# Optimization experiments

Hardware: AMD Instinct MI355X
Metric: run time of the kernel (lower is better)

The kernel has to match this reference:

```python
import jax, jax.numpy as jnp
import numpy as np

B, S, D, H, F = 2, 1024, 2048, 16, 8192
DH = D // H
MAX_ALPHA = 0.2
CN_SCALE = D / (D - 1)  # CenterNorm scale factor dim/(dim-1)


def setup_inputs() -> dict:
    key = jax.random.key(0)
    ks = jax.random.split(key, 8)
    s = 0.02
    f32 = jnp.float32
    return {
        "x": jax.random.normal(ks[0], (B, S, D), f32),
        "ln1_g": jnp.ones((D,), f32), "ln1_b": jnp.zeros((D,), f32),
        "wq": jax.random.normal(ks[1], (D, D), f32) * s, "bq": jnp.zeros((D,), f32),
        "wk": jax.random.normal(ks[2], (D, D), f32) * s, "bk": jnp.zeros((D,), f32),
        "wv": jax.random.normal(ks[3], (D, D), f32) * s, "bv": jnp.zeros((D,), f32),
        "wo": jax.random.normal(ks[4], (D, D), f32) * s, "bo": jnp.zeros((D,), f32),
        "tau": jnp.ones((H,), f32),   # learnable per-head temperature, init_tau=1.0
        "nu": jnp.ones((H,), f32),    # learnable per-head output scale, init_nu=1.0
        "alpha1": jnp.full((D,), 0.1, f32),  # per-channel residual weight, init 0.1
        "ln2_g": jnp.ones((D,), f32), "ln2_b": jnp.zeros((D,), f32),
        "w1": jax.random.normal(ks[5], (F, D), f32) * s, "b1": jnp.zeros((F,), f32),
        "w2": jax.random.normal(ks[6], (D, F), f32) * s, "b2": jnp.zeros((D,), f32),
        "alpha2": jnp.full((D,), 0.1, f32),
    }


def _center_norm(x, g, b):
    # CenterNorm: subtract mean only (no variance), scale by dim/(dim-1)
    mu = jnp.mean(x, axis=-1, keepdims=True)
    return g * (CN_SCALE * (x - mu)) + b


def _l2norm(t):
    return t / (jnp.linalg.norm(t, axis=-1, keepdims=True) + 1e-6)


def _cosine_attn(x, wq, bq, wk, bk, wv, bv, wo, bo, tau, nu):
    # project and split heads -> [B,H,S,DH]
    def proj(w, b):
        return (jnp.einsum('bsd,ed->bse', x, w) + b).reshape(B, S, H, DH).transpose(0, 2, 1, 3)
    q, k, v = proj(wq, bq), proj(wk, bk), proj(wv, bv)
    qn, kn = _l2norm(q), _l2norm(k)  # cosine similarity attention
    scores = jnp.einsum('bhqd,bhkd->bhqk', qn, kn) * tau[None, :, None, None]
    causal = jnp.tril(jnp.ones((S, S), bool))
    scores = jnp.where(causal[None, None], scores, -jnp.inf)
    p = jax.nn.softmax(scores, axis=-1)
    o = jnp.einsum('bhqk,bhkd->bhqd', p, v) * nu[None, :, None, None]
    o = o.transpose(0, 2, 1, 3).reshape(B, S, D)
    return jnp.einsum('bsd,ed->bse', o, wo) + bo


def _ffn(x, w1, b1, w2, b2):
    h = jax.nn.gelu(jnp.einsum('bsd,fd->bsf', x, w1) + b1)
    return jnp.einsum('bsf,df->bsd', h, w2) + b2


def reference(x, ln1_g, ln1_b, wq, bq, wk, bk, wv, bv, wo, bo, tau, nu,
              alpha1, ln2_g, ln2_b, w1, b1, w2, b2, alpha2):
    a = _center_norm(x, ln1_g, ln1_b)
    a1 = jnp.clip(alpha1, -MAX_ALPHA, MAX_ALPHA)
    x1 = a + a1 * _cosine_attn(a, wq, bq, wk, bk, wv, bv, wo, bo, tau, nu)
    m = _center_norm(x1, ln2_g, ln2_b)
    a2 = jnp.clip(alpha2, -MAX_ALPHA, MAX_ALPHA)
    return m + a2 * _ffn(m, w1, b1, w2, b2)
```

## Files before the change

### kernel.cpp

```cpp
#include <hip/hip_runtime.h>
#include <hip/hip_bf16.h>
#include <stdint.h>

#define B_ 2
#define S_ 1024
#define D_ 2048
#define H_ 16
#define F_ 8192
#define DH_ 128
#define M_ 2048

typedef unsigned short u16;
typedef __attribute__((ext_vector_type(8))) short short8;
typedef __attribute__((ext_vector_type(4))) float f32x4;
typedef __attribute__((ext_vector_type(2))) float f32x2;
typedef __attribute__((ext_vector_type(2))) unsigned short u16x2;

__device__ __forceinline__ u16 f2bf(float f) {
  union { float f; uint32_t u; } c; c.f = f;
  uint32_t r = c.u + 0x7FFFu + ((c.u >> 16) & 1u);
  return (u16)(r >> 16);
}

__device__ __forceinline__ void gload16(const void* g, void* l) {
  __builtin_amdgcn_global_load_lds((const __attribute__((address_space(1))) void*)g,
                                   (__attribute__((address_space(3))) void*)l, 16, 0, 0);
}

__device__ __forceinline__ float clipa(float a) {
  return fminf(0.2f, fmaxf(-0.2f, a));
}

__device__ __forceinline__ float gelu_f(float x) {
  float z = 0.7978845608028654f * (x + 0.044715f * x * x * x);
  z = fminf(10.f, fmaxf(-10.f, z));
  float e = __expf(2.f * z);
  return 0.5f * x * (1.f + (e - 1.f) / (e + 1.f));
}

__global__ __launch_bounds__(256) void k_cvt_all(const float* __restrict__ wq,
                                                 const float* __restrict__ wk,
                                                 const float* __restrict__ wv,
                                                 const float* __restrict__ wo,
                                                 const float* __restrict__ w1,
                                                 const float* __restrict__ w2,
                                                 u16* __restrict__ dst) {
  const int gi = blockIdx.x * 256 + threadIdx.x;
  const float* s;
  int off;
  if (gi < 2097152) {
    int r = gi >> 19;
    s = r == 0 ? wq : (r == 1 ? wk : (r == 2 ? wv : wo));
    off = gi & 524287;
  } else if (gi < 4194304) {
    s = w1; off = gi - 2097152;
  } else {
    s = w2; off = gi - 4194304;
  }
  f32x4 a = *(const f32x4*)(s + (size_t)off * 8);
  f32x4 b = *(const f32x4*)(s + (size_t)off * 8 + 4);
  short8 o;
  o[0] = (short)f2bf(a[0]); o[1] = (short)f2bf(a[1]);
  o[2] = (short)f2bf(a[2]); o[3] = (short)f2bf(a[3]);
  o[4] = (short)f2bf(b[0]); o[5] = (short)f2bf(b[1]);
  o[6] = (short)f2bf(b[2]); o[7] = (short)f2bf(b[3]);
  *(short8*)(dst + (size_t)gi * 8) = o;
}

__global__ __launch_bounds__(256) void k_centernorm(const float* __restrict__ x,
                                                    const float* __restrict__ g,
                                                    const float* __restrict__ bb,
                                                    float* __restrict__ of,
                                                    u16* __restrict__ ob) {
  const int row = blockIdx.x;
  const int t = threadIdx.x;
  const float* xr = x + (size_t)row * D_;
  f32x4 v0 = *(const f32x4*)(xr + t * 8);
  f32x4 v1 = *(const f32x4*)(xr + t * 8 + 4);
  float s = v0[0] + v0[1] + v0[2] + v0[3] + v1[0] + v1[1] + v1[2] + v1[3];
#pragma unroll
  for (int off = 1; off < 64; off <<= 1) s += __shfl_xor(s, off);
  __shared__ float red[4];
  if ((t & 63) == 0) red[t >> 6] = s;
  __syncthreads();
  const float mu = (red[0] + red[1] + red[2] + red[3]) * (1.0f / D_);
  const float CNS = (float)D_ / (float)(D_ - 1);
  f32x4 g0 = *(const f32x4*)(g + t * 8);
  f32x4 g1 = *(const f32x4*)(g + t * 8 + 4);
  f32x4 b0 = *(const f32x4*)(bb + t * 8);
  f32x4 b1 = *(const f32x4*)(bb + t * 8 + 4);
  f32x4 y0, y1;
  short8 yb;
#pragma unroll
  for (int i = 0; i < 4; i++) {
    y0[i] = g0[i] * (CNS * (v0[i] - mu)) + b0[i];
    y1[i] = g1[i] * (CNS * (v1[i] - mu)) + b1[i];
  }
#pragma unroll
  for (int i = 0; i < 4; i++) { yb[i] = (short)f2bf(y0[i]); yb[4 + i] = (short)f2bf(y1[i]); }
  float* orow = of + (size_t)row * D_;
  *(f32x4*)(orow + t * 8) = y0;
  *(f32x4*)(orow + t * 8 + 4) = y1;
  *(short8*)(ob + (size_t)row * D_ + t * 8) = yb;
}

__global__ __launch_bounds__(256) void k_l2norm(const float* __restrict__ q,
                                                const float* __restrict__ k,
                                                const float* __restrict__ v,
                                                u16* __restrict__ qn,
                                                u16* __restrict__ kn,
                                                u16* __restrict__ vn) {
  const int gw = blockIdx.x * 4 + (threadIdx.x >> 6);
  const int l = threadIdx.x & 63;
  const int h = gw & (H_ - 1);
  const int s = (gw >> 4) & (S_ - 1);
  const int b = gw >> 14;
  const size_t src = ((size_t)(b * S_ + s)) * D_ + h * DH_ + l * 2;
  const size_t dst = (((size_t)(b * H_ + h)) * S_ + s) * DH_ + l * 2;
  {
    f32x2 xv = *(const f32x2*)(q + src);
    float ss = xv[0] * xv[0] + xv[1] * xv[1];
#pragma unroll
    for (int off = 1; off < 64; off <<= 1) ss += __shfl_xor(ss, off);
    float sc = 1.f / (sqrtf(ss) + 1e-6f);
    u16x2 o; o[0] = f2bf(xv[0] * sc); o[1] = f2bf(xv[1] * sc);
    *(u16x2*)(qn + dst) = o;
  }
  {
    f32x2 xv = *(const f32x2*)(k + src);
    float ss = xv[0] * xv[0] + xv[1] * xv[1];
#pragma unroll
    for (int off = 1; off < 64; off <<= 1) ss += __shfl_xor(ss, off);
    float sc = 1.f / (sqrtf(ss) + 1e-6f);
    u16x2 o; o[0] = f2bf(xv[0] * sc); o[1] = f2bf(xv[1] * sc);
    *(u16x2*)(kn + dst) = o;
  }
  {
    f32x2 xv = *(const f32x2*)(v + src);
    u16x2 o; o[0] = f2bf(xv[0]); o[1] = f2bf(xv[1]);
    *(u16x2*)(vn + dst) = o;
  }
}

template <int EPI>
__device__ __forceinline__ void gemm256_core(const u16* __restrict__ A,
                                             const u16* __restrict__ Bt,
                                             const float* __restrict__ bias,
                                             float* __restrict__ outf,
                                             u16* __restrict__ outb,
                                             int N, int K, int kbase, int nk,
                                             int m0, int n0) {
  __shared__ char lds[2][65536];
  const int t = threadIdx.x;
  const int l = t & 63, w = t >> 6;
  const int wr = w >> 2, wc = w & 3;
  const int l15 = l & 15, lhi = l >> 4;
  const int sw = (l15 & 7) << 4;
  const int ab0 = l15 * 128 + ((lhi * 16) ^ sw);
  const int ab1 = l15 * 128 + ((64 + lhi * 16) ^ sw);

  auto stage = [&](int kt, int h) {
#pragma unroll
    for (int rj = 0; rj < 4; rj++) {
      const int region = rj >> 1, j = rj & 1;
      const int pl = h * 16384 + j * 8192 + t * 16;
      const int row = pl >> 7;
      const int scol = (pl & 127) ^ ((row & 7) << 4);
      const int grow = (region ? n0 : m0) + row;
      const char* src = (const char*)(region ? Bt : A) +
                        (size_t)grow * (size_t)(K * 2) +
                        (size_t)((kbase + kt * 64) * 2 + scol);
      gload16(src, &lds[kt & 1][region * 32768 + pl]);
    }
  };

  f32x4 acc[8][4] = {};

  stage(0, 0); stage(0, 1); stage(1, 0);
  asm volatile("s_waitcnt vmcnt(4)" ::: "memory");
  __builtin_amdgcn_s_barrier();
  __builtin_amdgcn_sched_barrier(0);

  for (int kt = 0; kt < nk; ++kt) {
    const char* base = &lds[kt & 1][0];
    const char* pA0 = base + wr * 4096 + ab0;
    const char* pA1 = base + wr * 4096 + ab1;
    const char* pB0 = base + 32768 + wc * 8192 + ab0;
    const char* pB1 = base + 32768 + wc * 8192 + ab1;
    short8 bf[4][2];
#pragma unroll
    for (int ni = 0; ni < 4; ni++) {
      bf[ni][0] = *(const short8*)(pB0 + ni * 2048);
      bf[ni][1] = *(const short8*)(pB1 + ni * 2048);
    }
#pragma unroll
    for (int q = 0; q < 4; q++) {
      short8 aq[2][2];
#pragma unroll
      for (int mi = 0; mi < 2; mi++) {
        aq[mi][0] = *(const short8*)(pA0 + q * 8192 + mi * 2048);
        aq[mi][1] = *(const short8*)(pA1 + q * 8192 + mi * 2048);
      }
      if (q == 1 && kt + 1 < nk) stage(kt + 1, 1);
      if (q == 3 && kt + 2 < nk) stage(kt + 2, 0);
      __builtin_amdgcn_s_setprio(1);
#pragma unroll
      for (int ks = 0; ks < 2; ks++)
#pragma unroll
        for (int mi = 0; mi < 2; mi++)
#pragma unroll
          for (int ni = 0; ni < 4; ni++)
            acc[q * 2 + mi][ni] = __builtin_amdgcn_mfma_f32_16x16x32_bf16(
                aq[mi][ks], bf[ni][ks], acc[q * 2 + mi][ni], 0, 0, 0);
      __builtin_amdgcn_s_setprio(0);
      if (q == 1) __builtin_amdgcn_s_barrier();
    }
    if (kt + 1 < nk) {
      if (kt + 2 < nk) { asm volatile("s_waitcnt vmcnt(4)" ::: "memory"); }
      else             { asm volatile("s_waitcnt vmcnt(0)" ::: "memory"); }
      __builtin_amdgcn_s_barrier();
      __builtin_amdgcn_sched_barrier(0);
    }
  }

#pragma unroll
  for (int ni = 0; ni < 4; ni++) {
    const int col = n0 + wc * 64 + ni * 16 + l15;
    const float bcol = (EPI == 3) ? 0.f : bias[col];
#pragma unroll
    for (int ai = 0; ai < 8; ai++) {
      const int row = m0 + (ai >> 1) * 64 + wr * 32 + (ai & 1) * 16 + lhi * 4;
#pragma unroll
      for (int j = 0; j < 4; j++) {
        const float v = acc[ai][ni][j] + bcol;
        const size_t idx = (size_t)(row + j) * N + col;
        if (EPI == 0) outf[idx] = v;
        else if (EPI == 2) outb[idx] = f2bf(gelu_f(v));
        else outf[idx] = v;
      }
    }
  }
}

__global__ __launch_bounds__(512, 2) void k_qkv256(const u16* A, const u16* W,
                                                   const float* b0, const float* b1,
                                                   const float* b2, float* o0, float* o1,
                                                   float* o2) {
  const int z = blockIdx.z;
  const u16* Bt = W + (size_t)z * 4194304;
  const float* bias = z == 0 ? b0 : (z == 1 ? b1 : b2);
  float* out = z == 0 ? o0 : (z == 1 ? o1 : o2);
  gemm256_core<0>(A, Bt, bias, out, nullptr, D_, D_, 0, 32,
                  blockIdx.y * 256, blockIdx.x * 256);
}

__global__ __launch_bounds__(512, 2) void k_ffn1_256(const u16* A, const u16* Bt,
                                                     const float* bias, u16* outb) {
  gemm256_core<2>(A, Bt, bias, nullptr, outb, F_, D_, 0, 32,
                  blockIdx.y * 256, blockIdx.x * 256);
}

__global__ __launch_bounds__(512, 2) void k_ffn2_256(const u16* A, const u16* Bt, float* P) {
  gemm256_core<3>(A, Bt, nullptr, P + (size_t)blockIdx.z * M_ * D_, nullptr, D_, F_,
                  blockIdx.z * 2048, 32, blockIdx.y * 256, blockIdx.x * 256);
}

__device__ __forceinline__ void gemm128_res(const u16* __restrict__ A,
                                            const u16* __restrict__ Bt,
                                            const float* __restrict__ bias,
                                            const float* __restrict__ res,
                                            const float* __restrict__ alpha,
                                            float* __restrict__ outf, int N, int K) {
  __shared__ u16 As[2][128 * 32];
  __shared__ u16 Bs[2][128 * 32];
  const int t = threadIdx.x;
  const int l = t & 63;
  const int w = t >> 6;
  const int wr = w >> 1, wc = w & 1;
  const int l15 = l & 15, lhi = l >> 4;
  const int m0 = blockIdx.y * 128, n0 = blockIdx.x * 128;
  f32x4 acc[4][4] = {};
  const int srow = t >> 2;
  const int scol = (t & 3) * 8;
  const u16* Ag = A + (size_t)(m0 + srow) * K + scol;
  const u16* Ag2 = Ag + (size_t)64 * K;
  const u16* Bg = Bt + (size_t)(n0 + srow) * K + scol;
  const u16* Bg2 = Bg + (size_t)64 * K;
  const int loff = t * 16;
  const int kiters = K / 32;

  gload16(Ag, (char*)As[0] + loff);
  gload16(Ag2, (char*)As[0] + 4096 + loff);
  gload16(Bg, (char*)Bs[0] + loff);
  gload16(Bg2, (char*)Bs[0] + 4096 + loff);
  __syncthreads();

  int cur = 0;
  for (int it = 0; it < kiters; ++it) {
    if (it + 1 < kiters) {
      const int k0 = (it + 1) * 32;
      char* dA = (char*)As[cur ^ 1] + loff;
      char* dB = (char*)Bs[cur ^ 1] + loff;
      gload16(Ag + k0, dA);
      gload16(Ag2 + k0, dA + 4096);
      gload16(Bg + k0, dB);
      gload16(Bg2 + k0, dB + 4096);
    }
    short8 af[4], bfr[4];
#pragma unroll
    for (int i = 0; i < 4; i++)
      af[i] = *(const short8*)(As[cur] + (wr * 64 + i * 16 + l15) * 32 + lhi * 8);
#pragma unroll
    for (int i = 0; i < 4; i++)
      bfr[i] = *(const short8*)(Bs[cur] + (wc * 64 + i * 16 + l15) * 32 + lhi * 8);
#pragma unroll
    for (int mi = 0; mi < 4; mi++)
#pragma unroll
      for (int ni = 0; ni < 4; ni++)
        acc[mi][ni] = __builtin_amdgcn_mfma_f32_16x16x32_bf16(af[mi], bfr[ni], acc[mi][ni], 0, 0, 0);
    __syncthreads();
    cur ^= 1;
  }
#pragma unroll
  for (int ni = 0; ni < 4; ni++) {
    const int col = n0 + wc * 64 + ni * 16 + l15;
    const float bcol = bias[col];
    const float alc = clipa(alpha[col]);
#pragma unroll
    for (int mi = 0; mi < 4; mi++) {
#pragma unroll
      for (int j = 0; j < 4; j++) {
        const int row = m0 + wr * 64 + mi * 16 + lhi * 4 + j;
        const size_t idx = (size_t)row * N + col;
        outf[idx] = res[idx] + alc * (acc[mi][ni][j] + bcol);
      }
    }
  }
}

__global__ __launch_bounds__(256) void k_oproj(const u16* A, const u16* Bt, const float* bias,
                                               const float* res, const float* alpha,
                                               float* outf) {
  gemm128_res(A, Bt, bias, res, alpha, outf, D_, D_);
}

__global__ __launch_bounds__(256) void k_ffn2_combine(const float* __restrict__ P,
                                                      const float* __restrict__ bias,
                                                      const float* __restrict__ res,
                                                      const float* __restrict__ alpha,
                                                      float* __restrict__ out) {
  const int i = blockIdx.x * 256 + threadIdx.x;
  const size_t base = (size_t)i * 8;
  const int col = (int)(base & (D_ - 1));
  const size_t PS = (size_t)M_ * D_;
  f32x4 s0 = {}, s1 = {};
#pragma unroll
  for (int p = 0; p < 4; p++) {
    s0 += *(const f32x4*)(P + p * PS + base);
    s1 += *(const f32x4*)(P + p * PS + base + 4);
  }
  f32x4 b0 = *(const f32x4*)(bias + col);
  f32x4 b1 = *(const f32x4*)(bias + col + 4);
  f32x4 a0 = *(const f32x4*)(alpha + col);
  f32x4 a1 = *(const f32x4*)(alpha + col + 4);
  f32x4 r0 = *(const f32x4*)(res + base);
  f32x4 r1 = *(const f32x4*)(res + base + 4);
  f32x4 o0, o1;
#pragma unroll
  for (int j = 0; j < 4; j++) {
    o0[j] = r0[j] + clipa(a0[j]) * (s0[j] + b0[j]);
    o1[j] = r1[j] + clipa(a1[j]) * (s1[j] + b1[j]);
  }
  *(f32x4*)(out + base) = o0;
  *(f32x4*)(out + base + 4) = o1;
}

__global__ __launch_bounds__(256) void k_attn(const u16* __restrict__ qn,
                                              const u16* __restrict__ kn,
                                              const u16* __restrict__ vn,
                                              const float* __restrict__ tau,
                                              const float* __restrict__ nu,
                                              u16* __restrict__ o) {
  __shared__ u16 Ks[64 * 128];
  __shared__ u16 Vt[128 * 64];
  __shared__ u16 Pl[4][16][72];
  const int t = threadIdx.x;
  const int l = t & 63, w = t >> 6;
  const int l15 = l & 15, lhi = l >> 4;
  const int qt = blockIdx.x;
  const int bh = blockIdx.y;
  const int h = bh & (H_ - 1);
  const int b = bh >> 4;
  const size_t hoff = (size_t)bh * S_ * DH_;
  const u16* Qh = qn + hoff;
  const u16* Kh = kn + hoff;
  const u16* Vh = vn + hoff;
  const int q0 = qt * 64;
  const int r0 = q0 + w * 16;
  short8 qf[4];
#pragma unroll
  for (int kk = 0; kk < 4; kk++)
    qf[kk] = *(const short8*)(Qh + (size_t)(r0 + l15) * DH_ + kk * 32 + lhi * 8);
  const float taum = tau[h];
  float mrow[4], lrow[4];
  f32x4 oacc[8] = {};
#pragma unroll
  for (int j = 0; j < 4; j++) { mrow[j] = -1e30f; lrow[j] = 0.f; }

  for (int kv0 = 0; kv0 < q0 + 64; kv0 += 64) {
#pragma unroll
    for (int i = 0; i < 4; i++) {
      const int p = i * 4096 + t * 16;
      const int row = p >> 8;
      const int colb = p & 255;
      const int scolb = colb ^ ((row & 7) << 4);
      gload16((const char*)(Kh + (size_t)(kv0 + row) * DH_) + scolb, (char*)Ks + p);
    }
#pragma unroll
    for (int i = 0; i < 4; i++) {
      const int c0 = w * 8 + i * 32;
      const int r = l;
      short8 vv = *(const short8*)(Vh + (size_t)(kv0 + r) * DH_ + c0);
#pragma unroll
      for (int j = 0; j < 8; j++) {
        const int ba = ((c0 + j) * 128 + r * 2) ^ (((c0 + j) & 7) << 4);
        *(u16*)((char*)Vt + ba) = (u16)vv[j];
      }
    }
    __syncthreads();
    f32x4 st[4] = {};
#pragma unroll
    for (int ks = 0; ks < 4; ks++) {
#pragma unroll
      for (int ct = 0; ct < 4; ct++) {
        const int n = ct * 16 + l15;
        const int ka = (ks * 32 + lhi * 8) * 2;
        short8 kf = *(const short8*)((const char*)Ks + n * 256 + (ka ^ ((n & 7) << 4)));
        st[ct] = __builtin_amdgcn_mfma_f32_16x16x32_bf16(qf[ks], kf, st[ct], 0, 0, 0);
      }
    }
    float pm[4] = {-1e30f, -1e30f, -1e30f, -1e30f};
#pragma unroll
    for (int ct = 0; ct < 4; ct++) {
      const int col = kv0 + ct * 16 + l15;
#pragma unroll
      for (int j = 0; j < 4; j++) {
        const int row = r0 + lhi * 4 + j;
        float s = st[ct][j] * taum;
        s = (col <= row) ? s : -1e30f;
        st[ct][j] = s;
        pm[j] = fmaxf(pm[j], s);
      }
    }
#pragma unroll
    for (int j = 0; j < 4; j++) {
#pragma unroll
      for (int off = 1; off < 16; off <<= 1) pm[j] = fmaxf(pm[j], __shfl_xor(pm[j], off));
    }
    float scl[4], psum[4];
#pragma unroll
    for (int j = 0; j < 4; j++) {
      const float nm = fmaxf(mrow[j], pm[j]);
      scl[j] = __expf(mrow[j] - nm);
      mrow[j] = nm;
      psum[j] = 0.f;
    }
#pragma unroll
    for (int ct = 0; ct < 4; ct++) {
#pragma unroll
      for (int j = 0; j < 4; j++) {
        const float p = __expf(st[ct][j] - mrow[j]);
        psum[j] += p;
        Pl[w][lhi * 4 + j][ct * 16 + l15] = f2bf(p);
      }
    }
#pragma unroll
    for (int j = 0; j < 4; j++) {
#pragma unroll
      for (int off = 1; off < 16; off <<= 1) psum[j] += __shfl_xor(psum[j], off);
      lrow[j] = lrow[j] * scl[j] + psum[j];
    }
#pragma unroll
    for (int nt = 0; nt < 8; nt++) {
#pragma unroll
      for (int j = 0; j < 4; j++) oacc[nt][j] *= scl[j];
    }
#pragma unroll
    for (int ks2 = 0; ks2 < 2; ks2++) {
      short8 pa = *(const short8*)((const char*)&Pl[w][0][0] + l15 * 144 + ks2 * 64 + lhi * 16);
#pragma unroll
      for (int nt = 0; nt < 8; nt++) {
        const int n = nt * 16 + l15;
        const int ba = (n * 128 + (ks2 * 32 + lhi * 8) * 2) ^ ((n & 7) << 4);
        short8 vf = *(const short8*)((const char*)Vt + ba);
        oacc[nt] = __builtin_amdgcn_mfma_f32_16x16x32_bf16(pa, vf, oacc[nt], 0, 0, 0);
      }
    }
    __syncthreads();
  }
  const float num = nu[h];
  float rs[4];
#pragma unroll
  for (int j = 0; j < 4; j++) rs[j] = num / lrow[j];
#pragma unroll
  for (int nt = 0; nt < 8; nt++) {
    const int col = h * DH_ + nt * 16 + l15;
#pragma unroll
    for (int j = 0; j < 4; j++) {
      const int row = r0 + lhi * 4 + j;
      o[((size_t)b * S_ + row) * D_ + col] = f2bf(oacc[nt][j] * rs[j]);
    }
  }
}

extern "C" void kernel_launch(void* const* d_in, const int* in_sizes, int n_in,
                              void* d_out, int out_size, void* d_ws, size_t ws_size,
                              hipStream_t stream) {
  const float* x    = (const float*)d_in[0];
  const float* ln1g = (const float*)d_in[1];
  const float* ln1b = (const float*)d_in[2];
  const float* wq   = (const float*)d_in[3];
  const float* bq   = (const float*)d_in[4];
  const float* wk   = (const float*)d_in[5];
  const float* bk   = (const float*)d_in[6];
  const float* wv   = (const float*)d_in[7];
  const float* bv   = (const float*)d_in[8];
  const float* wo   = (const float*)d_in[9];
  const float* bo   = (const float*)d_in[10];
  const float* tau  = (const float*)d_in[11];
  const float* nu   = (const float*)d_in[12];
  const float* al1  = (const float*)d_in[13];
  const float* ln2g = (const float*)d_in[14];
  const float* ln2b = (const float*)d_in[15];
  const float* w1   = (const float*)d_in[16];
  const float* b1   = (const float*)d_in[17];
  const float* w2   = (const float*)d_in[18];
  const float* b2   = (const float*)d_in[19];
  const float* al2  = (const float*)d_in[20];

  char* ws = (char*)d_ws;
  u16* WQ = (u16*)(ws + 0);
  u16* WO = (u16*)(ws + 25165824);
  u16* W1B = (u16*)(ws + 33554432);
  u16* W2B = (u16*)(ws + 67108864);
  float* AF = (float*)(ws + 100663296);
  u16*   AB = (u16*)(ws + 117440512);
  float* QF = (float*)(ws + 125829120);
  float* KF = (float*)(ws + 142606336);
  float* VF = (float*)(ws + 159383552);
  u16* QN = (u16*)(ws + 176160768);
  u16* KN = (u16*)(ws + 184549376);
  u16* VN = (u16*)(ws + 192937984);
  u16*   OB = (u16*)(ws + 125829120);
  u16*   MB = (u16*)(ws + 134217728);
  float* X1 = (float*)(ws + 142606336);
  float* MF2 = (float*)(ws + 159383552);
  u16*   HB = (u16*)(ws + 176160768);
  float* P4 = (float*)(ws + 0);

  k_cvt_all<<<24576, 256, 0, stream>>>(wq, wk, wv, wo, w1, w2, WQ);

  k_centernorm<<<M_, 256, 0, stream>>>(x, ln1g, ln1b, AF, AB);

  k_qkv256<<<dim3(8, 8, 3), 512, 0, stream>>>(AB, WQ, bq, bk, bv, QF, KF, VF);

  k_l2norm<<<8192, 256, 0, stream>>>(QF, KF, VF, QN, KN, VN);

  k_attn<<<dim3(S_ / 64, B_ * H_), 256, 0, stream>>>(QN, KN, VN, tau, nu, OB);

  k_oproj<<<dim3(16, 16), 256, 0, stream>>>(OB, WO, bo, AF, al1, X1);

  k_centernorm<<<M_, 256, 0, stream>>>(X1, ln2g, ln2b, MF2, MB);

  k_ffn1_256<<<dim3(32, 8), 512, 0, stream>>>(MB, W1B, b1, HB);

  k_ffn2_256<<<dim3(8, 8, 4), 512, 0, stream>>>(HB, W2B, P4);
  k_ffn2_combine<<<2048, 256, 0, stream>>>(P4, b2, MF2, al2, (float*)d_out);
}
```

Measured before the change: 399.7 us.

## Fuse L2-norm, tau scaling and head transpose into QKV GEMM epilogue

```diff
diff --git a/kernel.cpp b/kernel.cpp
--- a/kernel.cpp
+++ b/kernel.cpp
@@ -14,12 +14,16 @@
 typedef __attribute__((ext_vector_type(8))) short short8;
 typedef __attribute__((ext_vector_type(4))) float f32x4;
 typedef __attribute__((ext_vector_type(2))) float f32x2;
-typedef __attribute__((ext_vector_type(2))) unsigned short u16x2;
 
 __device__ __forceinline__ u16 f2bf(float f) {
   union { float f; uint32_t u; } c; c.f = f;
   uint32_t r = c.u + 0x7FFFu + ((c.u >> 16) & 1u);
   return (u16)(r >> 16);
+}
+
+__device__ __forceinline__ float bf2f(u16 v) {
+  union { uint32_t u; float f; } c; c.u = ((uint32_t)v) << 16;
+  return c.f;
 }
 
 __device__ __forceinline__ void gload16(const void* g, void* l) {
@@ -45,26 +49,28 @@
                                                  const float* __restrict__ w1,
                                                  const float* __restrict__ w2,
                                                  u16* __restrict__ dst) {
-  const int gi = blockIdx.x * 256 + threadIdx.x;
-  const float* s;
-  int off;
-  if (gi < 2097152) {
-    int r = gi >> 19;
-    s = r == 0 ? wq : (r == 1 ? wk : (r == 2 ? wv : wo));
-    off = gi & 524287;
-  } else if (gi < 4194304) {
-    s = w1; off = gi - 2097152;
-  } else {
-    s = w2; off = gi - 4194304;
-  }
-  f32x4 a = *(const f32x4*)(s + (size_t)off * 8);
-  f32x4 b = *(const f32x4*)(s + (size_t)off * 8 + 4);
-  short8 o;
-  o[0] = (short)f2bf(a[0]); o[1] = (short)f2bf(a[1]);
-  o[2] = (short)f2bf(a[2]); o[3] = (short)f2bf(a[3]);
-  o[4] = (short)f2bf(b[0]); o[5] = (short)f2bf(b[1]);
-  o[6] = (short)f2bf(b[2]); o[7] = (short)f2bf(b[3]);
-  *(short8*)(dst + (size_t)gi * 8) = o;
+  const int tot = 6291456;
+  for (int gi = blockIdx.x * 256 + threadIdx.x; gi < tot; gi += 2048 * 256) {
+    const float* s;
+    int off;
+    if (gi < 2097152) {
+      int r = gi >> 19;
+      s = r == 0 ? wq : (r == 1 ? wk : (r == 2 ? wv : wo));
+      off = gi & 524287;
+    } else if (gi < 4194304) {
+      s = w1; off = gi - 2097152;
+    } else {
+      s = w2; off = gi - 4194304;
+    }
+    f32x4 a = *(const f32x4*)(s + (size_t)off * 8);
+    f32x4 b = *(const f32x4*)(s + (size_t)off * 8 + 4);
+    short8 o;
+    o[0] = (short)f2bf(a[0]); o[1] = (short)f2bf(a[1]);
+    o[2] = (short)f2bf(a[2]); o[3] = (short)f2bf(a[3]);
+    o[4] = (short)f2bf(b[0]); o[5] = (short)f2bf(b[1]);
+    o[6] = (short)f2bf(b[2]); o[7] = (short)f2bf(b[3]);
+    *(short8*)(dst + (size_t)gi * 8) = o;
+  }
 }
 
 __global__ __launch_bounds__(256) void k_centernorm(const float* __restrict__ x,
@@ -104,44 +110,6 @@
   *(short8*)(ob + (size_t)row * D_ + t * 8) = yb;
 }
 
-__global__ __launch_bounds__(256) void k_l2norm(const float* __restrict__ q,
-                                                const float* __restrict__ k,
-                                                const float* __restrict__ v,
-                                                u16* __restrict__ qn,
-                                                u16* __restrict__ kn,
-                                                u16* __restrict__ vn) {
-  const int gw = blockIdx.x * 4 + (threadIdx.x >> 6);
-  const int l = threadIdx.x & 63;
-  const int h = gw & (H_ - 1);
-  const int s = (gw >> 4) & (S_ - 1);
-  const int b = gw >> 14;
-  const size_t src = ((size_t)(b * S_ + s)) * D_ + h * DH_ + l * 2;
-  const size_t dst = (((size_t)(b * H_ + h)) * S_ + s) * DH_ + l * 2;
-  {
-    f32x2 xv = *(const f32x2*)(q + src);
-    float ss = xv[0] * xv[0] + xv[1] * xv[1];
-#pragma unroll
-    for (int off = 1; off < 64; off <<= 1) ss += __shfl_xor(ss, off);
-    float sc = 1.f / (sqrtf(ss) + 1e-6f);
-    u16x2 o; o[0] = f2bf(xv[0] * sc); o[1] = f2bf(xv[1] * sc);
-    *(u16x2*)(qn + dst) = o;
-  }
-  {
-    f32x2 xv = *(const f32x2*)(k + src);
-    float ss = xv[0] * xv[0] + xv[1] * xv[1];
-#pragma unroll
-    for (int off = 1; off < 64; off <<= 1) ss += __shfl_xor(ss, off);
-    float sc = 1.f / (sqrtf(ss) + 1e-6f);
-    u16x2 o; o[0] = f2bf(xv[0] * sc); o[1] = f2bf(xv[1] * sc);
-    *(u16x2*)(kn + dst) = o;
-  }
-  {
-    f32x2 xv = *(const f32x2*)(v + src);
-    u16x2 o; o[0] = f2bf(xv[0]); o[1] = f2bf(xv[1]);
-    *(u16x2*)(vn + dst) = o;
-  }
-}
-
 template <int EPI>
 __device__ __forceinline__ void gemm256_core(const u16* __restrict__ A,
                                              const u16* __restrict__ Bt,
@@ -149,7 +117,9 @@
                                              float* __restrict__ outf,
                                              u16* __restrict__ outb,
                                              int N, int K, int kbase, int nk,
-                                             int m0, int n0) {
+                                             int m0, int n0,
+                                             const float* __restrict__ tau,
+                                             u16* __restrict__ qkv, int z) {
   __shared__ char lds[2][65536];
   const int t = threadIdx.x;
   const int l = t & 63, w = t >> 6;
@@ -223,6 +193,75 @@
     }
   }
 
+  if constexpr (EPI == 4) {
+    __shared__ float part[4][256];
+#pragma unroll
+    for (int ni = 0; ni < 4; ni++) {
+      const float bc = bias[n0 + wc * 64 + ni * 16 + l15];
+#pragma unroll
+      for (int ai = 0; ai < 8; ai++)
+#pragma unroll
+        for (int j = 0; j < 4; j++) acc[ai][ni][j] += bc;
+    }
+    if (z < 2) {
+      float p[8][4];
+#pragma unroll
+      for (int ai = 0; ai < 8; ai++)
+#pragma unroll
+        for (int j = 0; j < 4; j++) {
+          p[ai][j] = acc[ai][0][j] * acc[ai][0][j] + acc[ai][1][j] * acc[ai][1][j] +
+                     acc[ai][2][j] * acc[ai][2][j] + acc[ai][3][j] * acc[ai][3][j];
+#pragma unroll
+          for (int off = 1; off < 16; off <<= 1) p[ai][j] += __shfl_xor(p[ai][j], off);
+        }
+      if (l15 == 0) {
+#pragma unroll
+        for (int ai = 0; ai < 8; ai++)
+#pragma unroll
+          for (int j = 0; j < 4; j++) {
+            const int rb = (ai >> 1) * 64 + wr * 32 + (ai & 1) * 16 + lhi * 4 + j;
+            part[wc][rb] = p[ai][j];
+          }
+      }
+    }
+    __syncthreads();
+    const int hl = wc >> 1;
+    const int hglob = (n0 >> 7) + hl;
+    const float tauh = (z == 0) ? tau[hglob] : 1.f;
+    char* yt = (char*)&lds[0][0] + w * 16384;
+#pragma unroll
+    for (int ai = 0; ai < 8; ai++) {
+#pragma unroll
+      for (int j = 0; j < 4; j++) {
+        float sc = 1.f;
+        if (z < 2) {
+          const int rb = (ai >> 1) * 64 + wr * 32 + (ai & 1) * 16 + lhi * 4 + j;
+          const float ssq = part[2 * hl][rb] + part[2 * hl + 1][rb];
+          sc = tauh / (sqrtf(ssq) + 1e-6f);
+        }
+        const int rl = (ai >> 1) * 32 + (ai & 1) * 16 + lhi * 4 + j;
+        const int swz = (rl & 7) << 4;
+#pragma unroll
+        for (int ni = 0; ni < 4; ni++) {
+          const int cbyte = (ni * 16 + l15) * 2;
+          *(u16*)(yt + rl * 128 + (cbyte ^ swz)) = f2bf(acc[ai][ni][j] * sc);
+        }
+      }
+    }
+    __syncthreads();
+#pragma unroll
+    for (int pass = 0; pass < 16; pass++) {
+      const int rl = pass * 8 + (l >> 3);
+      const int cb = (l & 7) * 16;
+      const short8 v = *(const short8*)(yt + rl * 128 + (cb ^ ((rl & 7) << 4)));
+      const int m = m0 + ((rl >> 5) << 6) + wr * 32 + (rl & 31);
+      const int bb2 = m >> 10, s = m & 1023;
+      const int d = (wc & 1) * 64 + (cb >> 1);
+      *(short8*)(qkv + (((size_t)(bb2 * H_ + hglob)) * S_ + s) * DH_ + d) = v;
+    }
+    return;
+  }
+
 #pragma unroll
   for (int ni = 0; ni < 4; ni++) {
     const int col = n0 + wc * 64 + ni * 16 + l15;
@@ -236,7 +275,7 @@
         const size_t idx = (size_t)(row + j) * N + col;
         if (EPI == 0) outf[idx] = v;
         else if (EPI == 2) outb[idx] = f2bf(gelu_f(v));
-        else outf[idx] = v;
+        else outb[idx] = f2bf(v);
       }
     }
   }
@@ -244,25 +283,26 @@
 
 __global__ __launch_bounds__(512, 2) void k_qkv256(const u16* A, const u16* W,
                                                    const float* b0, const float* b1,
-                                                   const float* b2, float* o0, float* o1,
-                                                   float* o2) {
+                                                   const float* b2, const float* tau,
+                                                   u16* qn, u16* kn, u16* vn) {
   const int z = blockIdx.z;
   const u16* Bt = W + (size_t)z * 4194304;
   const float* bias = z == 0 ? b0 : (z == 1 ? b1 : b2);
-  float* out = z == 0 ? o0 : (z == 1 ? o1 : o2);
-  gemm256_core<0>(A, Bt, bias, out, nullptr, D_, D_, 0, 32,
-                  blockIdx.y * 256, blockIdx.x * 256);
+  u16* dst = z == 0 ? qn : (z == 1 ? kn : vn);
+  gemm256_core<4>(A, Bt, bias, nullptr, nullptr, D_, D_, 0, 32,
+                  blockIdx.y * 256, blockIdx.x * 256, tau, dst, z);
 }
 
 __global__ __launch_bounds__(512, 2) void k_ffn1_256(const u16* A, const u16* Bt,
                                                      const float* bias, u16* outb) {
   gemm256_core<2>(A, Bt, bias, nullptr, outb, F_, D_, 0, 32,
-                  blockIdx.y * 256, blockIdx.x * 256);
-}
-
-__global__ __launch_bounds__(512, 2) void k_ffn2_256(const u16* A, const u16* Bt, float* P) {
-  gemm256_core<3>(A, Bt, nullptr, P + (size_t)blockIdx.z * M_ * D_, nullptr, D_, F_,
-                  blockIdx.z * 2048, 32, blockIdx.y * 256, blockIdx.x * 256);
+                  blockIdx.y * 256, blockIdx.x * 256, nullptr, nullptr, 0);
+}
+
+__global__ __launch_bounds__(512, 2) void k_ffn2_256(const u16* A, const u16* Bt, u16* P) {
+  gemm256_core<3>(A, Bt, nullptr, nullptr, P + (size_t)blockIdx.z * M_ * D_, D_, F_,
+                  blockIdx.z * 2048, 32, blockIdx.y * 256, blockIdx.x * 256,
+                  nullptr, nullptr, 0);
 }
 
 __device__ __forceinline__ void gemm128_res(const u16* __restrict__ A,
@@ -344,7 +384,7 @@
   gemm128_res(A, Bt, bias, res, alpha, outf, D_, D_);
 }
 
-__global__ __launch_bounds__(256) void k_ffn2_combine(const float* __restrict__ P,
+__global__ __launch_bounds__(256) void k_ffn2_combine(const u16* __restrict__ P,
                                                       const float* __restrict__ bias,
                                                       const float* __restrict__ res,
                                                       const float* __restrict__ alpha,
@@ -353,11 +393,12 @@
   const size_t base = (size_t)i * 8;
   const int col = (int)(base & (D_ - 1));
   const size_t PS = (size_t)M_ * D_;
-  f32x4 s0 = {}, s1 = {};
+  float s[8] = {};
 #pragma unroll
   for (int p = 0; p < 4; p++) {
-    s0 += *(const f32x4*)(P + p * PS + base);
-    s1 += *(const f32x4*)(P + p * PS + base + 4);
+    short8 v = *(const short8*)(P + p * PS + base);
+#pragma unroll
+    for (int j = 0; j < 8; j++) s[j] += bf2f((u16)v[j]);
   }
   f32x4 b0 = *(const f32x4*)(bias + col);
   f32x4 b1 = *(const f32x4*)(bias + col + 4);
@@ -368,8 +409,8 @@
   f32x4 o0, o1;
 #pragma unroll
   for (int j = 0; j < 4; j++) {
-    o0[j] = r0[j] + clipa(a0[j]) * (s0[j] + b0[j]);
-    o1[j] = r1[j] + clipa(a1[j]) * (s1[j] + b1[j]);
+    o0[j] = r0[j] + clipa(a0[j]) * (s[j] + b0[j]);
+    o1[j] = r1[j] + clipa(a1[j]) * (s[4 + j] + b1[j]);
   }
   *(f32x4*)(out + base) = o0;
   *(f32x4*)(out + base + 4) = o1;
@@ -378,7 +419,6 @@
 __global__ __launch_bounds__(256) void k_attn(const u16* __restrict__ qn,
                                               const u16* __restrict__ kn,
                                               const u16* __restrict__ vn,
-                                              const float* __restrict__ tau,
                                               const float* __restrict__ nu,
                                               u16* __restrict__ o) {
   __shared__ u16 Ks[64 * 128];
@@ -401,7 +441,6 @@
 #pragma unroll
   for (int kk = 0; kk < 4; kk++)
     qf[kk] = *(const short8*)(Qh + (size_t)(r0 + l15) * DH_ + kk * 32 + lhi * 8);
-  const float taum = tau[h];
   float mrow[4], lrow[4];
   f32x4 oacc[8] = {};
 #pragma unroll
@@ -446,7 +485,7 @@
 #pragma unroll
       for (int j = 0; j < 4; j++) {
         const int row = r0 + lhi * 4 + j;
-        float s = st[ct][j] * taum;
+        float s = st[ct][j];
         s = (col <= row) ? s : -1e30f;
         st[ct][j] = s;
         pm[j] = fmaxf(pm[j], s);
@@ -545,28 +584,23 @@
   u16* W2B = (u16*)(ws + 67108864);
   float* AF = (float*)(ws + 100663296);
   u16*   AB = (u16*)(ws + 117440512);
-  float* QF = (float*)(ws + 125829120);
-  float* KF = (float*)(ws + 142606336);
-  float* VF = (float*)(ws + 159383552);
-  u16* QN = (u16*)(ws + 176160768);
-  u16* KN = (u16*)(ws + 184549376);
-  u16* VN = (u16*)(ws + 192937984);
   u16*   OB = (u16*)(ws + 125829120);
   u16*   MB = (u16*)(ws + 134217728);
   float* X1 = (float*)(ws + 142606336);
   float* MF2 = (float*)(ws + 159383552);
+  u16* QN = (u16*)(ws + 176160768);
+  u16* KN = (u16*)(ws + 184549376);
+  u16* VN = (u16*)(ws + 192937984);
   u16*   HB = (u16*)(ws + 176160768);
-  float* P4 = (float*)(ws + 0);
-
-  k_cvt_all<<<24576, 256, 0, stream>>>(wq, wk, wv, wo, w1, w2, WQ);
+  u16*   P4 = (u16*)(ws + 0);
+
+  k_cvt_all<<<2048, 256, 0, stream>>>(wq, wk, wv, wo, w1, w2, WQ);
 
   k_centernorm<<<M_, 256, 0, stream>>>(x, ln1g, ln1b, AF, AB);
 
-  k_qkv256<<<dim3(8, 8, 3), 512, 0, stream>>>(AB, WQ, bq, bk, bv, QF, KF, VF);
-
-  k_l2norm<<<8192, 256, 0, stream>>>(QF, KF, VF, QN, KN, VN);
-
-  k_attn<<<dim3(S_ / 64, B_ * H_), 256, 0, stream>>>(QN, KN, VN, tau, nu, OB);
+  k_qkv256<<<dim3(8, 8, 3), 512, 0, stream>>>(AB, WQ, bq, bk, bv, tau, QN, KN, VN);
+
+  k_attn<<<dim3(S_ / 64, B_ * H_), 256, 0, stream>>>(QN, KN, VN, nu, OB);
 
   k_oproj<<<dim3(16, 16), 256, 0, stream>>>(OB, WO, bo, AF, al1, X1);
 
```

New measurement: 409.1 us. 2.3% more time.
